# Performance work log

Measured on AMD Instinct MI355X. Metric: run time of the kernel, lower is better.

## Reference

```python
import jax, jax.numpy as jnp
import numpy as np

B, C, H_IMG, W_LEN = 32, 32, 16, 512
IN_CH = C * H_IMG          # 512, LSTM input size
OUT_CH = 1024              # bidirectional output size
HID = OUT_CH // 2          # 512, hidden per direction


def setup_inputs() -> dict:
    key = jax.random.key(0)
    ks = jax.random.split(key, 9)
    s = 1.0 / np.sqrt(HID)  # torch LSTM default init scale
    u = lambda k, shape: jax.random.uniform(k, shape, jnp.float32, -s, s)
    return {
        "x": jax.random.normal(ks[0], (B, C, H_IMG, W_LEN), jnp.float32),
        "W_ih_f": u(ks[1], (4 * HID, IN_CH)),
        "W_hh_f": u(ks[2], (4 * HID, HID)),
        "b_ih_f": u(ks[3], (4 * HID,)),
        "b_hh_f": u(ks[4], (4 * HID,)),
        "W_ih_b": u(ks[5], (4 * HID, IN_CH)),
        "W_hh_b": u(ks[6], (4 * HID, HID)),
        "b_ih_b": u(ks[7], (4 * HID,)),
        "b_hh_b": u(ks[8], (4 * HID,)),
    }


def _lstm_dir(x, W_ih, W_hh, b_ih, b_hh, reverse):
    # x: [B, T, IN] -> h sequence [B, T, HID]; torch gate order (i, f, g, o)
    xp = jnp.einsum('bti,gi->btg', x, W_ih) + b_ih + b_hh  # input proj for all steps
    xp = jnp.swapaxes(xp, 0, 1)  # [T, B, 4H]
    if reverse:
        xp = xp[::-1]
    h0 = jnp.zeros((x.shape[0], HID), x.dtype)

    def step(carry, xp_t):
        h, c = carry
        g = xp_t + h @ W_hh.T
        i, f, gg, o = jnp.split(g, 4, axis=-1)
        c = jax.nn.sigmoid(f) * c + jax.nn.sigmoid(i) * jnp.tanh(gg)
        h = jax.nn.sigmoid(o) * jnp.tanh(c)
        return (h, c), h

    _, hs = jax.lax.scan(step, (h0, h0), xp)  # hs: [T, B, HID]
    if reverse:
        hs = hs[::-1]
    return jnp.swapaxes(hs, 0, 1)  # [B, T, HID]


def reference(x, W_ih_f, W_hh_f, b_ih_f, b_hh_f, W_ih_b, W_hh_b, b_ih_b, b_hh_b):
    Bn, Cn, Hn, Wn = x.shape
    # permute(0,3,1,2).view(B, W, C*H): width is the time axis
    xs = jnp.transpose(x, (0, 3, 1, 2)).reshape(Bn, Wn, Cn * Hn)
    hf = _lstm_dir(xs, W_ih_f, W_hh_f, b_ih_f, b_hh_f, reverse=False)
    hb = _lstm_dir(xs, W_ih_b, W_hh_b, b_ih_b, b_hh_b, reverse=True)
    out = jnp.concatenate([hf, hb], axis=-1)        # [B, W, OUT]
    out = jnp.swapaxes(out, 1, 2)                    # [B, OUT, W]
    return out.reshape(Bn, -1, Hn, Wn)               # [B, OUT//H, H, W]
```

## Files before the change

### kernel.cpp

```cpp
#include <hip/hip_runtime.h>
#include <hip/hip_bf16.h>

#define BATCH 32
#define TLEN 512
#define INCH 512
#define HID 512

typedef __bf16 bf16x8 __attribute__((ext_vector_type(8)));
typedef float f32x4 __attribute__((ext_vector_type(4)));
typedef unsigned short u16x4 __attribute__((ext_vector_type(4)));
using bf16 = __hip_bfloat16;

#define OFF_XS2   0ull
#define OFF_WCAT  16777216ull
#define OFF_WHHP  20971520ull
#define OFF_BIAS  25165824ull
#define OFF_HBUF  25182208ull
#define OFF_CTR   25313280ull
#define OFF_FLAG  25313536ull
#define OFF_XP    25321728ull
#define WS_REQUIRED (25321728ull + 134217728ull)

__device__ __forceinline__ float sigmoid_fast(float x) {
    return 1.f / (1.f + __expf(-x));
}
__device__ __forceinline__ float tanh_fast(float x) {
    float ax = fabsf(x);
    float e = __expf(-2.f * ax);
    float r = (1.f - e) / (1.f + e);
    return copysignf(r, x);
}
__device__ __forceinline__ float bf2f(unsigned short u) {
    unsigned int i = ((unsigned int)u) << 16;
    float f; __builtin_memcpy(&f, &i, 4); return f;
}

__global__ void ws_too_small_kernel(float* out) {
    if (threadIdx.x == 0 && blockIdx.x == 0) out[0] = 12345.0f;
}

__global__ void pack_x_kernel(const float* __restrict__ x, bf16* __restrict__ XS2) {
    int bx = blockIdx.x;
    int b  = bx >> 6;
    int tt = (bx >> 3) & 7;
    int kt = bx & 7;
    __shared__ float tile[64][65];
    int tid  = threadIdx.x;
    int row2 = tid >> 6;
    int col  = tid & 63;
#pragma unroll
    for (int i = 0; i < 16; ++i) {
        int row = i * 4 + row2;
        int k = kt * 64 + row;
        tile[row][col] = x[((b * 32 + (k >> 4)) * 16 + (k & 15)) * 512 + tt * 64 + col];
    }
    __syncthreads();
#pragma unroll
    for (int i = 0; i < 16; ++i) {
        int trow = i * 4 + row2;
        int t = tt * 64 + trow;
        XS2[(t * 32 + b) * 512 + kt * 64 + col] = __float2bfloat16(tile[col][trow]);
    }
}

__global__ void pack_w_kernel(const float* __restrict__ Wih_f, const float* __restrict__ Whh_f,
                              const float* __restrict__ bih_f, const float* __restrict__ bhh_f,
                              const float* __restrict__ Wih_b, const float* __restrict__ Whh_b,
                              const float* __restrict__ bih_b, const float* __restrict__ bhh_b,
                              bf16* __restrict__ Wcat, bf16* __restrict__ Whhp,
                              float* __restrict__ bias, unsigned int* __restrict__ hbuf32,
                              unsigned int* __restrict__ ctr, unsigned int* __restrict__ flags) {
    long idx = (long)blockIdx.x * 256 + threadIdx.x;
    if (idx < 262144) {
        long e = idx * 8;
        int m = (int)(e >> 9), k = (int)(e & 511);
        const float* src = (m < 2048) ? &Wih_f[(long)m * 512 + k]
                                      : &Wih_b[(long)(m - 2048) * 512 + k];
        bf16* dst = &Wcat[e];
#pragma unroll
        for (int j = 0; j < 8; ++j) dst[j] = __float2bfloat16(src[j]);
        return;
    }
    idx -= 262144;
    if (idx < 262144) {
        long e = idx * 8;
        int k  = (int)(e & 511);
        int lm = (int)((e >> 9) & 63);
        int s  = (int)((e >> 15) & 31);
        int dir = (int)(e >> 20);
        int grow = (lm & 3) * 512 + s * 16 + (lm >> 2);
        const float* W = dir ? Whh_b : Whh_f;
        const float* src = &W[(long)grow * 512 + k];
        bf16* dst = &Whhp[e];
#pragma unroll
        for (int j = 0; j < 8; ++j) dst[j] = __float2bfloat16(src[j]);
        return;
    }
    idx -= 262144;
    if (idx < 4096) {
        int dir  = (int)(idx >> 11);
        int r    = (int)(idx & 2047);
        int s    = r >> 6, ul = (r >> 2) & 15, gate = r & 3;
        int g    = gate * 512 + s * 16 + ul;
        bias[idx] = (dir ? (bih_b[g] + bhh_b[g]) : (bih_f[g] + bhh_f[g]));
        return;
    }
    idx -= 4096;
    if (idx < 32768) { hbuf32[idx] = 0u; return; }
    idx -= 32768;
    if (idx < 64) { ctr[idx] = 0u; return; }
    idx -= 64;
    if (idx < 2048) { flags[idx] = 0u; return; }
}

__global__ __launch_bounds__(256, 2) void gemm_xp_kernel(const bf16* __restrict__ Wcat,
                                                         const bf16* __restrict__ XS2,
                                                         bf16* __restrict__ XP) {
    int bm = (blockIdx.x & 31) * 128;
    int bn = (blockIdx.x >> 5) * 128;
    __shared__ bf16 lA[128 * 40];
    __shared__ bf16 lB[128 * 40];
    int tid = threadIdx.x;
    int lane = tid & 63, w = tid >> 6;
    int wm = (w & 1) * 64, wn = (w >> 1) * 64;
    int fr = lane & 15, fq = lane >> 4;
    f32x4 acc[4][4] = {};
    int r = tid >> 2, c = tid & 3;
    for (int kt = 0; kt < 16; ++kt) {
        int k0 = kt * 32;
        *(bf16x8*)&lA[r * 40 + c * 8]        = *(const bf16x8*)&Wcat[(long)(bm + r) * 512 + k0 + c * 8];
        *(bf16x8*)&lA[(r + 64) * 40 + c * 8] = *(const bf16x8*)&Wcat[(long)(bm + r + 64) * 512 + k0 + c * 8];
        *(bf16x8*)&lB[r * 40 + c * 8]        = *(const bf16x8*)&XS2[(long)(bn + r) * 512 + k0 + c * 8];
        *(bf16x8*)&lB[(r + 64) * 40 + c * 8] = *(const bf16x8*)&XS2[(long)(bn + r + 64) * 512 + k0 + c * 8];
        __syncthreads();
        bf16x8 af[4], bfm[4];
#pragma unroll
        for (int i = 0; i < 4; ++i) af[i]  = *(const bf16x8*)&lA[(wm + i * 16 + fr) * 40 + fq * 8];
#pragma unroll
        for (int i = 0; i < 4; ++i) bfm[i] = *(const bf16x8*)&lB[(wn + i * 16 + fr) * 40 + fq * 8];
#pragma unroll
        for (int mi = 0; mi < 4; ++mi)
#pragma unroll
            for (int ni = 0; ni < 4; ++ni)
                acc[mi][ni] = __builtin_amdgcn_mfma_f32_16x16x32_bf16(af[mi], bfm[ni], acc[mi][ni], 0, 0, 0);
        __syncthreads();
    }
#pragma unroll
    for (int mi = 0; mi < 4; ++mi) {
#pragma unroll
        for (int rr = 0; rr < 4; ++rr) {
            int m = bm + wm + mi * 16 + fq * 4 + rr;
            int dir = m >> 11, cc = m & 2047;
            int gate = cc >> 9, u = cc & 511, s = u >> 4, ul = u & 15;
#pragma unroll
            for (int ni = 0; ni < 4; ++ni) {
                int n = bn + wn + ni * 16 + fr;
                int t = n >> 5, b = n & 31;
                long off = ((long)(t * 2 + dir) * 32 + s) * 2048 + (long)(ul * 32 + b) * 4 + gate;
                XP[off] = __float2bfloat16(acc[mi][ni][rr]);
            }
        }
    }
}

__global__ __launch_bounds__(512, 2) void lstm_rec_kernel(const bf16* __restrict__ Whhp,
                                                          const bf16* __restrict__ XP,
                                                          const float* __restrict__ bias,
                                                          bf16* hbuf, float* out,
                                                          unsigned int* flags) {
    int bx = blockIdx.x;
    int dir = bx >> 5, s = bx & 31;
    int tid = threadIdx.x;
    int lane = tid & 63, w = tid >> 6;
    int mt = w & 3, nt = w >> 2;
    int fr = lane & 15, fq = lane >> 4;
    __shared__ float obuf[16][512];
    __shared__ bf16  hstage[BATCH * 16];
    __shared__ bf16  hsh[32 * 520];
    __shared__ int   eps;

    const bf16* wbase = Whhp + ((long)((dir * 32 + s) * 64 + mt * 16 + fr)) * 512 + fq * 8;
    bf16x8 wA[16];
#pragma unroll
    for (int kt = 0; kt < 16; ++kt) wA[kt] = *(const bf16x8*)(wbase + kt * 32);

    int ul = mt * 4 + fq;
    int b  = nt * 16 + fr;
    f32x4 bv = *(const f32x4*)&bias[((dir * 32 + s) * 16 + ul) * 4];
    float cstate = 0.f;

    bf16* hb_dir = hbuf + (long)dir * 2 * 16384;
    unsigned int* myflag = flags + (dir * 32 + s) * 32;
    const unsigned int* pollflag = flags + (dir * 32 + (lane & 31)) * 32;
    float* outrow = out + (long)b * 524288 + (long)(dir * 512 + s * 16 + ul) * 512;
    int c0 = tid * 4;
    int sb0 = ((c0 >> 1) & 31) * 520 + (c0 >> 6) * 16;
    int sb1 = (((c0 + 2) >> 1) & 31) * 520 + (c0 >> 6) * 16;
    int guard = 1 << 21;

    if (tid == 0) eps = 0;
    __syncthreads();

    for (int t = 0; t < TLEN; ++t) {
        int ttime = dir ? (TLEN - 1 - t) : t;
        const bf16* xpp = XP + (long)(ttime * 2 + dir) * 65536 + s * 2048 + (ul * 32 + b) * 4;
        u16x4 xv = *(const u16x4*)xpp;

        if (t > 0) {
            if (w == 1) {
                unsigned int target = (unsigned int)t;
                for (;;) {
                    unsigned int v = __hip_atomic_load(pollflag, __ATOMIC_RELAXED,
                                                       __HIP_MEMORY_SCOPE_AGENT);
                    if (__all(v >= target)) break;
                    if (--guard <= 0) break;
                }
                if (lane == 0)
                    __hip_atomic_store(&eps, t, __ATOMIC_RELAXED,
                                       __HIP_MEMORY_SCOPE_WORKGROUP);
            } else {
                while (__hip_atomic_load(&eps, __ATOMIC_RELAXED,
                                         __HIP_MEMORY_SCOPE_WORKGROUP) < t) {
                    if (--guard <= 0) break;
                }
            }
        }

        {
            const bf16* src = hb_dir + (long)(t & 1) * 16384 + (long)tid * 32;
            f32x4 v0, v1, v2, v3;
            asm volatile(
                "global_load_dwordx4 %0, %4, off sc0 sc1\n\t"
                "global_load_dwordx4 %1, %4, off offset:16 sc0 sc1\n\t"
                "global_load_dwordx4 %2, %4, off offset:32 sc0 sc1\n\t"
                "global_load_dwordx4 %3, %4, off offset:48 sc0 sc1\n\t"
                "s_waitcnt vmcnt(0)"
                : "=&v"(v0), "=&v"(v1), "=&v"(v2), "=&v"(v3)
                : "v"(src) : "memory");
            bf16* d0 = &hsh[sb0];
            bf16* d1 = &hsh[sb1];
            *(f32x4*)(d0)     = v0;
            *(f32x4*)(d0 + 8) = v1;
            *(f32x4*)(d1)     = v2;
            *(f32x4*)(d1 + 8) = v3;
        }
        __syncthreads();

        f32x4 a0 = {}, a1 = {}, a2 = {}, a3 = {};
        const bf16* hrow = &hsh[(nt * 16 + fr) * 520 + fq * 8];
#pragma unroll
        for (int kt = 0; kt < 16; kt += 4) {
            bf16x8 h0 = *(const bf16x8*)(hrow + (kt + 0) * 32);
            bf16x8 h1 = *(const bf16x8*)(hrow + (kt + 1) * 32);
            bf16x8 h2 = *(const bf16x8*)(hrow + (kt + 2) * 32);
            bf16x8 h3 = *(const bf16x8*)(hrow + (kt + 3) * 32);
            a0 = __builtin_amdgcn_mfma_f32_16x16x32_bf16(wA[kt + 0], h0, a0, 0, 0, 0);
            a1 = __builtin_amdgcn_mfma_f32_16x16x32_bf16(wA[kt + 1], h1, a1, 0, 0, 0);
            a2 = __builtin_amdgcn_mfma_f32_16x16x32_bf16(wA[kt + 2], h2, a2, 0, 0, 0);
            a3 = __builtin_amdgcn_mfma_f32_16x16x32_bf16(wA[kt + 3], h3, a3, 0, 0, 0);
        }

        float gi = (a0[0] + a1[0]) + (a2[0] + a3[0]) + bv[0] + bf2f(xv.x);
        float gf = (a0[1] + a1[1]) + (a2[1] + a3[1]) + bv[1] + bf2f(xv.y);
        float gg = (a0[2] + a1[2]) + (a2[2] + a3[2]) + bv[2] + bf2f(xv.z);
        float go = (a0[3] + a1[3]) + (a2[3] + a3[3]) + bv[3] + bf2f(xv.w);
        float si = sigmoid_fast(gi), sf = sigmoid_fast(gf), so = sigmoid_fast(go);
        cstate = sf * cstate + si * tanh_fast(gg);
        float h = so * tanh_fast(cstate);

        hstage[b * 16 + ul] = __float2bfloat16(h);
        obuf[ttime & 15][tid] = h;
        __syncthreads();

        if (w == 0) {
            f32x4 hv = *(const f32x4*)&hstage[lane * 8];
            bf16* dst = hb_dir + (long)((t + 1) & 1) * 16384 + s * 512 + lane * 8;
            asm volatile("global_store_dwordx4 %0, %1, off sc0 sc1"
                         :: "v"(dst), "v"(hv) : "memory");
            asm volatile("s_waitcnt vmcnt(0)" ::: "memory");
            if (lane == 0)
                __hip_atomic_store(myflag, (unsigned int)(t + 1), __ATOMIC_RELAXED,
                                   __HIP_MEMORY_SCOPE_AGENT);
        }

        if ((t & 15) == 15) {
            int tb = ttime & ~15;
            float vals[16];
#pragma unroll
            for (int c = 0; c < 16; ++c) vals[c] = obuf[c][tid];
            float* op = outrow + tb;
#pragma unroll
            for (int c4 = 0; c4 < 4; ++c4)
                *(f32x4*)(op + c4 * 4) = *(f32x4*)&vals[c4 * 4];
        }
    }
}

extern "C" void kernel_launch(void* const* d_in, const int* in_sizes, int n_in,
                              void* d_out, int out_size, void* d_ws, size_t ws_size,
                              hipStream_t stream) {
    const float* x     = (const float*)d_in[0];
    const float* Wih_f = (const float*)d_in[1];
    const float* Whh_f = (const float*)d_in[2];
    const float* bih_f = (const float*)d_in[3];
    const float* bhh_f = (const float*)d_in[4];
    const float* Wih_b = (const float*)d_in[5];
    const float* Whh_b = (const float*)d_in[6];
    const float* bih_b = (const float*)d_in[7];
    const float* bhh_b = (const float*)d_in[8];
    float* out = (float*)d_out;

    if (ws_size < WS_REQUIRED) {
        ws_too_small_kernel<<<1, 64, 0, stream>>>(out);
        return;
    }

    char* ws = (char*)d_ws;
    bf16* XS2  = (bf16*)(ws + OFF_XS2);
    bf16* Wcat = (bf16*)(ws + OFF_WCAT);
    bf16* Whhp = (bf16*)(ws + OFF_WHHP);
    float* bias = (float*)(ws + OFF_BIAS);
    bf16* hbuf = (bf16*)(ws + OFF_HBUF);
    unsigned int* ctr   = (unsigned int*)(ws + OFF_CTR);
    unsigned int* flags = (unsigned int*)(ws + OFF_FLAG);
    bf16* XP   = (bf16*)(ws + OFF_XP);

    pack_x_kernel<<<2048, 256, 0, stream>>>(x, XS2);
    pack_w_kernel<<<2201, 256, 0, stream>>>(Wih_f, Whh_f, bih_f, bhh_f,
                                            Wih_b, Whh_b, bih_b, bhh_b,
                                            Wcat, Whhp, bias, (unsigned int*)hbuf, ctr, flags);
    gemm_xp_kernel<<<4096, 256, 0, stream>>>(Wcat, XS2, XP);
    lstm_rec_kernel<<<64, 512, 0, stream>>>(Whhp, XP, bias, hbuf, out, flags);
}
```

Measured before the change: 1.957 ms.

## Interleave forward and backward LSTM directions within each persistent workgroup

Merges the two direction workgroups into one, so 32 workgroups each keep both directions' recurrent weight slices in registers and alternate forward and backward steps. The goal is to hide each direction's cross-workgroup flag-polling latency behind the other direction's work, and to drop the single-wave poller plus LDS broadcast in favour of all waves polling directly. This doubles register use (launch bounds lowered to one block per SM) and LDS use. Each direction's steps are now serialized inside a single workgroup, which can lengthen the critical path if the overlap does not materialize.

```diff
diff --git a/kernel.cpp b/kernel.cpp
--- a/kernel.cpp
+++ b/kernel.cpp
@@ -163,135 +163,211 @@
     }
 }
 
-__global__ __launch_bounds__(512, 2) void lstm_rec_kernel(const bf16* __restrict__ Whhp,
+__global__ __launch_bounds__(512, 1) void lstm_rec_kernel(const bf16* __restrict__ Whhp,
                                                           const bf16* __restrict__ XP,
                                                           const float* __restrict__ bias,
                                                           bf16* hbuf, float* out,
                                                           unsigned int* flags) {
-    int bx = blockIdx.x;
-    int dir = bx >> 5, s = bx & 31;
+    int s = blockIdx.x;
     int tid = threadIdx.x;
     int lane = tid & 63, w = tid >> 6;
     int mt = w & 3, nt = w >> 2;
     int fr = lane & 15, fq = lane >> 4;
-    __shared__ float obuf[16][512];
-    __shared__ bf16  hstage[BATCH * 16];
-    __shared__ bf16  hsh[32 * 520];
-    __shared__ int   eps;
-
-    const bf16* wbase = Whhp + ((long)((dir * 32 + s) * 64 + mt * 16 + fr)) * 512 + fq * 8;
-    bf16x8 wA[16];
-#pragma unroll
-    for (int kt = 0; kt < 16; ++kt) wA[kt] = *(const bf16x8*)(wbase + kt * 32);
+    __shared__ float obuf[2][16][512];
+    __shared__ bf16  hstage[2][BATCH * 16];
+    __shared__ bf16  hsh[2][32 * 520];
+
+    const bf16* wbf = Whhp + ((long)((0 * 32 + s) * 64 + mt * 16 + fr)) * 512 + fq * 8;
+    const bf16* wbb = Whhp + ((long)((1 * 32 + s) * 64 + mt * 16 + fr)) * 512 + fq * 8;
+    bf16x8 wAf[16], wAb[16];
+#pragma unroll
+    for (int kt = 0; kt < 16; ++kt) wAf[kt] = *(const bf16x8*)(wbf + kt * 32);
+#pragma unroll
+    for (int kt = 0; kt < 16; ++kt) wAb[kt] = *(const bf16x8*)(wbb + kt * 32);
 
     int ul = mt * 4 + fq;
     int b  = nt * 16 + fr;
-    f32x4 bv = *(const f32x4*)&bias[((dir * 32 + s) * 16 + ul) * 4];
-    float cstate = 0.f;
-
-    bf16* hb_dir = hbuf + (long)dir * 2 * 16384;
-    unsigned int* myflag = flags + (dir * 32 + s) * 32;
-    const unsigned int* pollflag = flags + (dir * 32 + (lane & 31)) * 32;
-    float* outrow = out + (long)b * 524288 + (long)(dir * 512 + s * 16 + ul) * 512;
+    f32x4 bvf = *(const f32x4*)&bias[((0 * 32 + s) * 16 + ul) * 4];
+    f32x4 bvb = *(const f32x4*)&bias[((1 * 32 + s) * 16 + ul) * 4];
+    float csf = 0.f, csb = 0.f;
+
+    bf16* hb_f = hbuf;
+    bf16* hb_b = hbuf + 2 * 16384;
+    unsigned int* myflag_f = flags + (0 * 32 + s) * 32;
+    unsigned int* myflag_b = flags + (1 * 32 + s) * 32;
+    const unsigned int* pollf = flags + (0 * 32 + (lane & 31)) * 32;
+    const unsigned int* pollb = flags + (1 * 32 + (lane & 31)) * 32;
+    float* outrow_f = out + (long)b * 524288 + (long)(0 * 512 + s * 16 + ul) * 512;
+    float* outrow_b = out + (long)b * 524288 + (long)(1 * 512 + s * 16 + ul) * 512;
     int c0 = tid * 4;
     int sb0 = ((c0 >> 1) & 31) * 520 + (c0 >> 6) * 16;
     int sb1 = (((c0 + 2) >> 1) & 31) * 520 + (c0 >> 6) * 16;
     int guard = 1 << 21;
 
-    if (tid == 0) eps = 0;
-    __syncthreads();
-
     for (int t = 0; t < TLEN; ++t) {
-        int ttime = dir ? (TLEN - 1 - t) : t;
-        const bf16* xpp = XP + (long)(ttime * 2 + dir) * 65536 + s * 2048 + (ul * 32 + b) * 4;
-        u16x4 xv = *(const u16x4*)xpp;
-
-        if (t > 0) {
-            if (w == 1) {
+        {
+            int ttime = t;
+            const bf16* xpp = XP + (long)(ttime * 2 + 0) * 65536 + s * 2048 + (ul * 32 + b) * 4;
+            u16x4 xv = *(const u16x4*)xpp;
+
+            if (t > 0) {
                 unsigned int target = (unsigned int)t;
                 for (;;) {
-                    unsigned int v = __hip_atomic_load(pollflag, __ATOMIC_RELAXED,
+                    unsigned int v = __hip_atomic_load(pollf, __ATOMIC_RELAXED,
                                                        __HIP_MEMORY_SCOPE_AGENT);
                     if (__all(v >= target)) break;
                     if (--guard <= 0) break;
                 }
+            }
+            {
+                const bf16* src = hb_f + (long)(t & 1) * 16384 + (long)tid * 32;
+                f32x4 v0, v1, v2, v3;
+                asm volatile(
+                    "global_load_dwordx4 %0, %4, off sc0 sc1\n\t"
+                    "global_load_dwordx4 %1, %4, off offset:16 sc0 sc1\n\t"
+                    "global_load_dwordx4 %2, %4, off offset:32 sc0 sc1\n\t"
+                    "global_load_dwordx4 %3, %4, off offset:48 sc0 sc1\n\t"
+                    "s_waitcnt vmcnt(0)"
+                    : "=&v"(v0), "=&v"(v1), "=&v"(v2), "=&v"(v3)
+                    : "v"(src) : "memory");
+                bf16* d0 = &hsh[0][sb0];
+                bf16* d1 = &hsh[0][sb1];
+                *(f32x4*)(d0)     = v0;
+                *(f32x4*)(d0 + 8) = v1;
+                *(f32x4*)(d1)     = v2;
+                *(f32x4*)(d1 + 8) = v3;
+            }
+            __syncthreads();
+
+            f32x4 a0 = {}, a1 = {}, a2 = {}, a3 = {};
+            const bf16* hrow = &hsh[0][(nt * 16 + fr) * 520 + fq * 8];
+#pragma unroll
+            for (int kt = 0; kt < 16; kt += 4) {
+                bf16x8 h0 = *(const bf16x8*)(hrow + (kt + 0) * 32);
+                bf16x8 h1 = *(const bf16x8*)(hrow + (kt + 1) * 32);
+                bf16x8 h2 = *(const bf16x8*)(hrow + (kt + 2) * 32);
+                bf16x8 h3 = *(const bf16x8*)(hrow + (kt + 3) * 32);
+                a0 = __builtin_amdgcn_mfma_f32_16x16x32_bf16(wAf[kt + 0], h0, a0, 0, 0, 0);
+                a1 = __builtin_amdgcn_mfma_f32_16x16x32_bf16(wAf[kt + 1], h1, a1, 0, 0, 0);
+                a2 = __builtin_amdgcn_mfma_f32_16x16x32_bf16(wAf[kt + 2], h2, a2, 0, 0, 0);
+                a3 = __builtin_amdgcn_mfma_f32_16x16x32_bf16(wAf[kt + 3], h3, a3, 0, 0, 0);
+            }
+            float gi = (a0[0] + a1[0]) + (a2[0] + a3[0]) + bvf[0] + bf2f(xv.x);
+            float gf = (a0[1] + a1[1]) + (a2[1] + a3[1]) + bvf[1] + bf2f(xv.y);
+            float gg = (a0[2] + a1[2]) + (a2[2] + a3[2]) + bvf[2] + bf2f(xv.z);
+            float go = (a0[3] + a1[3]) + (a2[3] + a3[3]) + bvf[3] + bf2f(xv.w);
+            float si = sigmoid_fast(gi), sf = sigmoid_fast(gf), so = sigmoid_fast(go);
+            csf = sf * csf + si * tanh_fast(gg);
+            float h = so * tanh_fast(csf);
+
+            hstage[0][b * 16 + ul] = __float2bfloat16(h);
+            obuf[0][ttime & 15][tid] = h;
+            __syncthreads();
+
+            if (w == 0) {
+                f32x4 hv = *(const f32x4*)&hstage[0][lane * 8];
+                bf16* dst = hb_f + (long)((t + 1) & 1) * 16384 + s * 512 + lane * 8;
+                asm volatile("global_store_dwordx4 %0, %1, off sc0 sc1"
+                             :: "v"(dst), "v"(hv) : "memory");
+                asm volatile("s_waitcnt vmcnt(0)" ::: "memory");
                 if (lane == 0)
-                    __hip_atomic_store(&eps, t, __ATOMIC_RELAXED,
-                                       __HIP_MEMORY_SCOPE_WORKGROUP);
-            } else {
-                while (__hip_atomic_load(&eps, __ATOMIC_RELAXED,
-                                         __HIP_MEMORY_SCOPE_WORKGROUP) < t) {
+                    __hip_atomic_store(myflag_f, (unsigned int)(t + 1), __ATOMIC_RELAXED,
+                                       __HIP_MEMORY_SCOPE_AGENT);
+            }
+        }
+
+        {
+            int ttime = TLEN - 1 - t;
+            const bf16* xpp = XP + (long)(ttime * 2 + 1) * 65536 + s * 2048 + (ul * 32 + b) * 4;
+            u16x4 xv = *(const u16x4*)xpp;
+
+            if (t > 0) {
+                unsigned int target = (unsigned int)t;
+                for (;;) {
+                    unsigned int v = __hip_atomic_load(pollb, __ATOMIC_RELAXED,
+                                                       __HIP_MEMORY_SCOPE_AGENT);
+                    if (__all(v >= target)) break;
                     if (--guard <= 0) break;
                 }
             }
+            {
+                const bf16* src = hb_b + (long)(t & 1) * 16384 + (long)tid * 32;
+                f32x4 v0, v1, v2, v3;
+                asm volatile(
+                    "global_load_dwordx4 %0, %4, off sc0 sc1\n\t"
+                    "global_load_dwordx4 %1, %4, off offset:16 sc0 sc1\n\t"
+                    "global_load_dwordx4 %2, %4, off offset:32 sc0 sc1\n\t"
+                    "global_load_dwordx4 %3, %4, off offset:48 sc0 sc1\n\t"
+                    "s_waitcnt vmcnt(0)"
+                    : "=&v"(v0), "=&v"(v1), "=&v"(v2), "=&v"(v3)
+                    : "v"(src) : "memory");
+                bf16* d0 = &hsh[1][sb0];
+                bf16* d1 = &hsh[1][sb1];
+                *(f32x4*)(d0)     = v0;
+                *(f32x4*)(d0 + 8) = v1;
+                *(f32x4*)(d1)     = v2;
+                *(f32x4*)(d1 + 8) = v3;
+            }
+            __syncthreads();
+
+            f32x4 a0 = {}, a1 = {}, a2 = {}, a3 = {};
+            const bf16* hrow = &hsh[1][(nt * 16 + fr) * 520 + fq * 8];
+#pragma unroll
+            for (int kt = 0; kt < 16; kt += 4) {
+                bf16x8 h0 = *(const bf16x8*)(hrow + (kt + 0) * 32);
+                bf16x8 h1 = *(const bf16x8*)(hrow + (kt + 1) * 32);
+                bf16x8 h2 = *(const bf16x8*)(hrow + (kt + 2) * 32);
+                bf16x8 h3 = *(const bf16x8*)(hrow + (kt + 3) * 32);
+                a0 = __builtin_amdgcn_mfma_f32_16x16x32_bf16(wAb[kt + 0], h0, a0, 0, 0, 0);
+                a1 = __builtin_amdgcn_mfma_f32_16x16x32_bf16(wAb[kt + 1], h1, a1, 0, 0, 0);
+                a2 = __builtin_amdgcn_mfma_f32_16x16x32_bf16(wAb[kt + 2], h2, a2, 0, 0, 0);
+                a3 = __builtin_amdgcn_mfma_f32_16x16x32_bf16(wAb[kt + 3], h3, a3, 0, 0, 0);
+            }
+            float gi = (a0[0] + a1[0]) + (a2[0] + a3[0]) + bvb[0] + bf2f(xv.x);
+            float gf = (a0[1] + a1[1]) + (a2[1] + a3[1]) + bvb[1] + bf2f(xv.y);
+            float gg = (a0[2] + a1[2]) + (a2[2] + a3[2]) + bvb[2] + bf2f(xv.z);
+            float go = (a0[3] + a1[3]) + (a2[3] + a3[3]) + bvb[3] + bf2f(xv.w);
+            float si = sigmoid_fast(gi), sf = sigmoid_fast(gf), so = sigmoid_fast(go);
+            csb = sf * csb + si * tanh_fast(gg);
+            float h = so * tanh_fast(csb);
+
+            hstage[1][b * 16 + ul] = __float2bfloat16(h);
+            obuf[1][ttime & 15][tid] = h;
+            __syncthreads();
+
+            if (w == 0) {
+                f32x4 hv = *(const f32x4*)&hstage[1][lane * 8];
+                bf16* dst = hb_b + (long)((t + 1) & 1) * 16384 + s * 512 + lane * 8;
+                asm volatile("global_store_dwordx4 %0, %1, off sc0 sc1"
+                             :: "v"(dst), "v"(hv) : "memory");
+                asm volatile("s_waitcnt vmcnt(0)" ::: "memory");
+                if (lane == 0)
+                    __hip_atomic_store(myflag_b, (unsigned int)(t + 1), __ATOMIC_RELAXED,
+                                       __HIP_MEMORY_SCOPE_AGENT);
+            }
         }
 
-        {
-            const bf16* src = hb_dir + (long)(t & 1) * 16384 + (long)tid * 32;
-            f32x4 v0, v1, v2, v3;
-            asm volatile(
-                "global_load_dwordx4 %0, %4, off sc0 sc1\n\t"
-                "global_load_dwordx4 %1, %4, off offset:16 sc0 sc1\n\t"
-                "global_load_dwordx4 %2, %4, off offset:32 sc0 sc1\n\t"
-                "global_load_dwordx4 %3, %4, off offset:48 sc0 sc1\n\t"
-                "s_waitcnt vmcnt(0)"
-                : "=&v"(v0), "=&v"(v1), "=&v"(v2), "=&v"(v3)
-                : "v"(src) : "memory");
-            bf16* d0 = &hsh[sb0];
-            bf16* d1 = &hsh[sb1];
-            *(f32x4*)(d0)     = v0;
-            *(f32x4*)(d0 + 8) = v1;
-            *(f32x4*)(d1)     = v2;
-            *(f32x4*)(d1 + 8) = v3;
-        }
-        __syncthreads();
-
-        f32x4 a0 = {}, a1 = {}, a2 = {}, a3 = {};
-        const bf16* hrow = &hsh[(nt * 16 + fr) * 520 + fq * 8];
-#pragma unroll
-        for (int kt = 0; kt < 16; kt += 4) {
-            bf16x8 h0 = *(const bf16x8*)(hrow + (kt + 0) * 32);
-            bf16x8 h1 = *(const bf16x8*)(hrow + (kt + 1) * 32);
-            bf16x8 h2 = *(const bf16x8*)(hrow + (kt + 2) * 32);
-            bf16x8 h3 = *(const bf16x8*)(hrow + (kt + 3) * 32);
-            a0 = __builtin_amdgcn_mfma_f32_16x16x32_bf16(wA[kt + 0], h0, a0, 0, 0, 0);
-            a1 = __builtin_amdgcn_mfma_f32_16x16x32_bf16(wA[kt + 1], h1, a1, 0, 0, 0);
-            a2 = __builtin_amdgcn_mfma_f32_16x16x32_bf16(wA[kt + 2], h2, a2, 0, 0, 0);
-            a3 = __builtin_amdgcn_mfma_f32_16x16x32_bf16(wA[kt + 3], h3, a3, 0, 0, 0);
-        }
-
-        float gi = (a0[0] + a1[0]) + (a2[0] + a3[0]) + bv[0] + bf2f(xv.x);
-        float gf = (a0[1] + a1[1]) + (a2[1] + a3[1]) + bv[1] + bf2f(xv.y);
-        float gg = (a0[2] + a1[2]) + (a2[2] + a3[2]) + bv[2] + bf2f(xv.z);
-        float go = (a0[3] + a1[3]) + (a2[3] + a3[3]) + bv[3] + bf2f(xv.w);
-        float si = sigmoid_fast(gi), sf = sigmoid_fast(gf), so = sigmoid_fast(go);
-        cstate = sf * cstate + si * tanh_fast(gg);
-        float h = so * tanh_fast(cstate);
-
-        hstage[b * 16 + ul] = __float2bfloat16(h);
-        obuf[ttime & 15][tid] = h;
-        __syncthreads();
-
-        if (w == 0) {
-            f32x4 hv = *(const f32x4*)&hstage[lane * 8];
-            bf16* dst = hb_dir + (long)((t + 1) & 1) * 16384 + s * 512 + lane * 8;
-            asm volatile("global_store_dwordx4 %0, %1, off sc0 sc1"
-                         :: "v"(dst), "v"(hv) : "memory");
-            asm volatile("s_waitcnt vmcnt(0)" ::: "memory");
-            if (lane == 0)
-                __hip_atomic_store(myflag, (unsigned int)(t + 1), __ATOMIC_RELAXED,
-                                   __HIP_MEMORY_SCOPE_AGENT);
-        }
-
         if ((t & 15) == 15) {
-            int tb = ttime & ~15;
-            float vals[16];
-#pragma unroll
-            for (int c = 0; c < 16; ++c) vals[c] = obuf[c][tid];
-            float* op = outrow + tb;
-#pragma unroll
-            for (int c4 = 0; c4 < 4; ++c4)
-                *(f32x4*)(op + c4 * 4) = *(f32x4*)&vals[c4 * 4];
+            {
+                int tb = t & ~15;
+                float vals[16];
+#pragma unroll
+                for (int c = 0; c < 16; ++c) vals[c] = obuf[0][c][tid];
+                float* op = outrow_f + tb;
+#pragma unroll
+                for (int c4 = 0; c4 < 4; ++c4)
+                    *(f32x4*)(op + c4 * 4) = *(f32x4*)&vals[c4 * 4];
+            }
+            {
+                int tb = (TLEN - 1 - t) & ~15;
+                float vals[16];
+#pragma unroll
+                for (int c = 0; c < 16; ++c) vals[c] = obuf[1][c][tid];
+                float* op = outrow_b + tb;
+#pragma unroll
+                for (int c4 = 0; c4 < 4; ++c4)
+                    *(f32x4*)(op + c4 * 4) = *(f32x4*)&vals[c4 * 4];
+            }
         }
     }
 }
@@ -330,5 +406,5 @@
                                             Wih_b, Whh_b, bih_b, bhh_b,
                                             Wcat, Whhp, bias, (unsigned int*)hbuf, ctr, flags);
     gemm_xp_kernel<<<4096, 256, 0, stream>>>(Wcat, XS2, XP);
-    lstm_rec_kernel<<<64, 512, 0, stream>>>(Whhp, XP, bias, hbuf, out, flags);
-}
+    lstm_rec_kernel<<<32, 512, 0, stream>>>(Whhp, XP, bias, hbuf, out, flags);
+}
```

Result: slower. 2.991 ms (+52.8%).

## Halve recurrent LSTM workgroups, each handling two hidden slices for all batches

Applied to the files above, without the earlier changes.

The persistent recurrent kernel drops from 64 to 32 workgroups. Each workgroup now covers two 16-unit hidden slices across the full batch, where before it covered one slice. Each wave keeps its weight fragment and issues two MFMA chains, one per 16-row batch half, instead of splitting the batch across waves. This halves the number of flags polled per step and the cross-workgroup synchronisation fan-in, in exchange for more per-workgroup work and LDS, and the larger obuf lowers the occupancy bound to one workgroup per CU.

```diff
diff --git a/kernel.cpp b/kernel.cpp
--- a/kernel.cpp
+++ b/kernel.cpp
@@ -163,19 +163,20 @@
     }
 }
 
-__global__ __launch_bounds__(512, 2) void lstm_rec_kernel(const bf16* __restrict__ Whhp,
+__global__ __launch_bounds__(512, 1) void lstm_rec_kernel(const bf16* __restrict__ Whhp,
                                                           const bf16* __restrict__ XP,
                                                           const float* __restrict__ bias,
                                                           bf16* hbuf, float* out,
                                                           unsigned int* flags) {
     int bx = blockIdx.x;
-    int dir = bx >> 5, s = bx & 31;
+    int dir = bx >> 4, blk = bx & 15;
     int tid = threadIdx.x;
     int lane = tid & 63, w = tid >> 6;
-    int mt = w & 3, nt = w >> 2;
+    int mt = w & 3, su = w >> 2;
     int fr = lane & 15, fq = lane >> 4;
-    __shared__ float obuf[16][512];
-    __shared__ bf16  hstage[BATCH * 16];
+    int s = blk * 2 + su;
+    __shared__ float obuf[16][1024];
+    __shared__ bf16  hstage[32 * 32];
     __shared__ bf16  hsh[32 * 520];
     __shared__ int   eps;
 
@@ -184,18 +185,17 @@
 #pragma unroll
     for (int kt = 0; kt < 16; ++kt) wA[kt] = *(const bf16x8*)(wbase + kt * 32);
 
-    int ul = mt * 4 + fq;
-    int b  = nt * 16 + fr;
-    f32x4 bv = *(const f32x4*)&bias[((dir * 32 + s) * 16 + ul) * 4];
-    float cstate = 0.f;
+    int ul16 = mt * 4 + fq;
+    int ul32 = su * 16 + ul16;
+    f32x4 bv = *(const f32x4*)&bias[((dir * 32 + s) * 16 + ul16) * 4];
+    float cs0 = 0.f, cs1 = 0.f;
 
     bf16* hb_dir = hbuf + (long)dir * 2 * 16384;
-    unsigned int* myflag = flags + (dir * 32 + s) * 32;
-    const unsigned int* pollflag = flags + (dir * 32 + (lane & 31)) * 32;
-    float* outrow = out + (long)b * 524288 + (long)(dir * 512 + s * 16 + ul) * 512;
-    int c0 = tid * 4;
-    int sb0 = ((c0 >> 1) & 31) * 520 + (c0 >> 6) * 16;
-    int sb1 = (((c0 + 2) >> 1) & 31) * 520 + (c0 >> 6) * 16;
+    unsigned int* myflag = flags + (dir * 16 + blk) * 32;
+    const unsigned int* pollflag = flags + (dir * 16 + (lane & 15)) * 32;
+    float* outrow0 = out + (long)fr * 524288 + (long)(dir * 512 + s * 16 + ul16) * 512;
+    float* outrow1 = outrow0 + 16l * 524288;
+    int sbo = (tid & 31) * 520 + (tid >> 5) * 32;
     int guard = 1 << 21;
 
     if (tid == 0) eps = 0;
@@ -203,8 +203,9 @@
 
     for (int t = 0; t < TLEN; ++t) {
         int ttime = dir ? (TLEN - 1 - t) : t;
-        const bf16* xpp = XP + (long)(ttime * 2 + dir) * 65536 + s * 2048 + (ul * 32 + b) * 4;
-        u16x4 xv = *(const u16x4*)xpp;
+        const bf16* xpp = XP + (long)(ttime * 2 + dir) * 65536 + s * 2048 + (ul16 * 32 + fr) * 4;
+        u16x4 xv0 = *(const u16x4*)xpp;
+        u16x4 xv1 = *(const u16x4*)(xpp + 64);
 
         if (t > 0) {
             if (w == 1) {
@@ -237,47 +238,59 @@
                 "s_waitcnt vmcnt(0)"
                 : "=&v"(v0), "=&v"(v1), "=&v"(v2), "=&v"(v3)
                 : "v"(src) : "memory");
-            bf16* d0 = &hsh[sb0];
-            bf16* d1 = &hsh[sb1];
-            *(f32x4*)(d0)     = v0;
-            *(f32x4*)(d0 + 8) = v1;
-            *(f32x4*)(d1)     = v2;
-            *(f32x4*)(d1 + 8) = v3;
+            bf16* d = &hsh[sbo];
+            *(f32x4*)(d)      = v0;
+            *(f32x4*)(d + 8)  = v1;
+            *(f32x4*)(d + 16) = v2;
+            *(f32x4*)(d + 24) = v3;
         }
         __syncthreads();
 
         f32x4 a0 = {}, a1 = {}, a2 = {}, a3 = {};
-        const bf16* hrow = &hsh[(nt * 16 + fr) * 520 + fq * 8];
-#pragma unroll
-        for (int kt = 0; kt < 16; kt += 4) {
-            bf16x8 h0 = *(const bf16x8*)(hrow + (kt + 0) * 32);
-            bf16x8 h1 = *(const bf16x8*)(hrow + (kt + 1) * 32);
-            bf16x8 h2 = *(const bf16x8*)(hrow + (kt + 2) * 32);
-            bf16x8 h3 = *(const bf16x8*)(hrow + (kt + 3) * 32);
-            a0 = __builtin_amdgcn_mfma_f32_16x16x32_bf16(wA[kt + 0], h0, a0, 0, 0, 0);
-            a1 = __builtin_amdgcn_mfma_f32_16x16x32_bf16(wA[kt + 1], h1, a1, 0, 0, 0);
-            a2 = __builtin_amdgcn_mfma_f32_16x16x32_bf16(wA[kt + 2], h2, a2, 0, 0, 0);
-            a3 = __builtin_amdgcn_mfma_f32_16x16x32_bf16(wA[kt + 3], h3, a3, 0, 0, 0);
-        }
-
-        float gi = (a0[0] + a1[0]) + (a2[0] + a3[0]) + bv[0] + bf2f(xv.x);
-        float gf = (a0[1] + a1[1]) + (a2[1] + a3[1]) + bv[1] + bf2f(xv.y);
-        float gg = (a0[2] + a1[2]) + (a2[2] + a3[2]) + bv[2] + bf2f(xv.z);
-        float go = (a0[3] + a1[3]) + (a2[3] + a3[3]) + bv[3] + bf2f(xv.w);
-        float si = sigmoid_fast(gi), sf = sigmoid_fast(gf), so = sigmoid_fast(go);
-        cstate = sf * cstate + si * tanh_fast(gg);
-        float h = so * tanh_fast(cstate);
-
-        hstage[b * 16 + ul] = __float2bfloat16(h);
-        obuf[ttime & 15][tid] = h;
+        const bf16* hrow0 = &hsh[fr * 520 + fq * 8];
+        const bf16* hrow1 = &hsh[(16 + fr) * 520 + fq * 8];
+#pragma unroll
+        for (int kt = 0; kt < 16; kt += 2) {
+            bf16x8 h00 = *(const bf16x8*)(hrow0 + (kt + 0) * 32);
+            bf16x8 h01 = *(const bf16x8*)(hrow0 + (kt + 1) * 32);
+            bf16x8 h10 = *(const bf16x8*)(hrow1 + (kt + 0) * 32);
+            bf16x8 h11 = *(const bf16x8*)(hrow1 + (kt + 1) * 32);
+            a0 = __builtin_amdgcn_mfma_f32_16x16x32_bf16(wA[kt + 0], h00, a0, 0, 0, 0);
+            a2 = __builtin_amdgcn_mfma_f32_16x16x32_bf16(wA[kt + 0], h10, a2, 0, 0, 0);
+            a1 = __builtin_amdgcn_mfma_f32_16x16x32_bf16(wA[kt + 1], h01, a1, 0, 0, 0);
+            a3 = __builtin_amdgcn_mfma_f32_16x16x32_bf16(wA[kt + 1], h11, a3, 0, 0, 0);
+        }
+
+        float gi0 = a0[0] + a1[0] + bv[0] + bf2f(xv0.x);
+        float gf0 = a0[1] + a1[1] + bv[1] + bf2f(xv0.y);
+        float gg0 = a0[2] + a1[2] + bv[2] + bf2f(xv0.z);
+        float go0 = a0[3] + a1[3] + bv[3] + bf2f(xv0.w);
+        float gi1 = a2[0] + a3[0] + bv[0] + bf2f(xv1.x);
+        float gf1 = a2[1] + a3[1] + bv[1] + bf2f(xv1.y);
+        float gg1 = a2[2] + a3[2] + bv[2] + bf2f(xv1.z);
+        float go1 = a2[3] + a3[3] + bv[3] + bf2f(xv1.w);
+        float si0 = sigmoid_fast(gi0), sf0 = sigmoid_fast(gf0), so0 = sigmoid_fast(go0);
+        float si1 = sigmoid_fast(gi1), sf1 = sigmoid_fast(gf1), so1 = sigmoid_fast(go1);
+        cs0 = sf0 * cs0 + si0 * tanh_fast(gg0);
+        cs1 = sf1 * cs1 + si1 * tanh_fast(gg1);
+        float h0 = so0 * tanh_fast(cs0);
+        float h1 = so1 * tanh_fast(cs1);
+
+        hstage[fr * 32 + ul32]        = __float2bfloat16(h0);
+        hstage[(fr + 16) * 32 + ul32] = __float2bfloat16(h1);
+        obuf[ttime & 15][tid]       = h0;
+        obuf[ttime & 15][tid + 512] = h1;
         __syncthreads();
 
         if (w == 0) {
-            f32x4 hv = *(const f32x4*)&hstage[lane * 8];
-            bf16* dst = hb_dir + (long)((t + 1) & 1) * 16384 + s * 512 + lane * 8;
-            asm volatile("global_store_dwordx4 %0, %1, off sc0 sc1"
-                         :: "v"(dst), "v"(hv) : "memory");
-            asm volatile("s_waitcnt vmcnt(0)" ::: "memory");
+            f32x4 hv0 = *(const f32x4*)&hstage[lane * 16];
+            f32x4 hv1 = *(const f32x4*)&hstage[lane * 16 + 8];
+            bf16* dst = hb_dir + (long)((t + 1) & 1) * 16384 + blk * 1024 + lane * 16;
+            asm volatile(
+                "global_store_dwordx4 %0, %2, off sc0 sc1\n\t"
+                "global_store_dwordx4 %1, %3, off sc0 sc1\n\t"
+                "s_waitcnt vmcnt(0)"
+                :: "v"(dst), "v"(dst + 8), "v"(hv0), "v"(hv1) : "memory");
             if (lane == 0)
                 __hip_atomic_store(myflag, (unsigned int)(t + 1), __ATOMIC_RELAXED,
                                    __HIP_MEMORY_SCOPE_AGENT);
@@ -288,7 +301,13 @@
             float vals[16];
 #pragma unroll
             for (int c = 0; c < 16; ++c) vals[c] = obuf[c][tid];
-            float* op = outrow + tb;
+            float* op = outrow0 + tb;
+#pragma unroll
+            for (int c4 = 0; c4 < 4; ++c4)
+                *(f32x4*)(op + c4 * 4) = *(f32x4*)&vals[c4 * 4];
+#pragma unroll
+            for (int c = 0; c < 16; ++c) vals[c] = obuf[c][tid + 512];
+            op = outrow1 + tb;
 #pragma unroll
             for (int c4 = 0; c4 < 4; ++c4)
                 *(f32x4*)(op + c4 * 4) = *(f32x4*)&vals[c4 * 4];
@@ -330,5 +349,5 @@
                                             Wih_b, Whh_b, bih_b, bhh_b,
                                             Wcat, Whhp, bias, (unsigned int*)hbuf, ctr, flags);
     gemm_xp_kernel<<<4096, 256, 0, stream>>>(Wcat, XS2, XP);
-    lstm_rec_kernel<<<64, 512, 0, stream>>>(Whhp, XP, bias, hbuf, out, flags);
-}
+    lstm_rec_kernel<<<32, 512, 0, stream>>>(Whhp, XP, bias, hbuf, out, flags);
+}
```

New measurement: 2.421 ms. 1.24x slower.

## Replace block barrier with per-slice LDS counters for fine-grained h dependency tracking

Applied to the files above, without the earlier changes.

Every thread now polls the global flag of the producer slice it loads instead of one wave polling all flags and broadcasting through LDS. The h tile is double-buffered in LDS, and per-slice workgroup-scope counters replace the __syncthreads before the MFMA loop. Each wave starts its K loop at a slice-dependent offset and waits only for the specific k-chunk it needs, so compute can begin as soon as the first producers' data arrive. This trades one barrier for many LDS atomic polls and more global polling traffic. Launch bounds change to one block per SM to make room for the doubled LDS.

```diff
diff --git a/kernel.cpp b/kernel.cpp
--- a/kernel.cpp
+++ b/kernel.cpp
@@ -163,7 +163,7 @@
     }
 }
 
-__global__ __launch_bounds__(512, 2) void lstm_rec_kernel(const bf16* __restrict__ Whhp,
+__global__ __launch_bounds__(512, 1) void lstm_rec_kernel(const bf16* __restrict__ Whhp,
                                                           const bf16* __restrict__ XP,
                                                           const float* __restrict__ bias,
                                                           bf16* hbuf, float* out,
@@ -176,8 +176,10 @@
     int fr = lane & 15, fq = lane >> 4;
     __shared__ float obuf[16][512];
     __shared__ bf16  hstage[BATCH * 16];
-    __shared__ bf16  hsh[32 * 520];
-    __shared__ int   eps;
+    __shared__ bf16  hsh[2][32 * 520];
+    __shared__ unsigned int scnt[2][32];
+
+    if (tid < 64) scnt[tid >> 5][tid & 31] = 0u;
 
     const bf16* wbase = Whhp + ((long)((dir * 32 + s) * 64 + mt * 16 + fr)) * 512 + fq * 8;
     bf16x8 wA[16];
@@ -191,43 +193,30 @@
 
     bf16* hb_dir = hbuf + (long)dir * 2 * 16384;
     unsigned int* myflag = flags + (dir * 32 + s) * 32;
-    const unsigned int* pollflag = flags + (dir * 32 + (lane & 31)) * 32;
+    int p = tid >> 4;
+    const unsigned int* pflag = flags + (dir * 32 + p) * 32;
     float* outrow = out + (long)b * 524288 + (long)(dir * 512 + s * 16 + ul) * 512;
     int c0 = tid * 4;
     int sb0 = ((c0 >> 1) & 31) * 520 + (c0 >> 6) * 16;
     int sb1 = (((c0 + 2) >> 1) & 31) * 520 + (c0 >> 6) * 16;
+    int kt_base = ((s >> 1) + 1) & 15;
     int guard = 1 << 21;
 
-    if (tid == 0) eps = 0;
     __syncthreads();
 
     for (int t = 0; t < TLEN; ++t) {
         int ttime = dir ? (TLEN - 1 - t) : t;
+        int buf = t & 1;
         const bf16* xpp = XP + (long)(ttime * 2 + dir) * 65536 + s * 2048 + (ul * 32 + b) * 4;
         u16x4 xv = *(const u16x4*)xpp;
 
-        if (t > 0) {
-            if (w == 1) {
-                unsigned int target = (unsigned int)t;
-                for (;;) {
-                    unsigned int v = __hip_atomic_load(pollflag, __ATOMIC_RELAXED,
-                                                       __HIP_MEMORY_SCOPE_AGENT);
-                    if (__all(v >= target)) break;
-                    if (--guard <= 0) break;
-                }
-                if (lane == 0)
-                    __hip_atomic_store(&eps, t, __ATOMIC_RELAXED,
-                                       __HIP_MEMORY_SCOPE_WORKGROUP);
-            } else {
-                while (__hip_atomic_load(&eps, __ATOMIC_RELAXED,
-                                         __HIP_MEMORY_SCOPE_WORKGROUP) < t) {
-                    if (--guard <= 0) break;
-                }
+        {
+            unsigned int target = (unsigned int)t;
+            while (__hip_atomic_load(pflag, __ATOMIC_RELAXED,
+                                     __HIP_MEMORY_SCOPE_AGENT) < target) {
+                if (--guard <= 0) break;
             }
-        }
-
-        {
-            const bf16* src = hb_dir + (long)(t & 1) * 16384 + (long)tid * 32;
+            const bf16* src = hb_dir + (long)buf * 16384 + (long)tid * 32;
             f32x4 v0, v1, v2, v3;
             asm volatile(
                 "global_load_dwordx4 %0, %4, off sc0 sc1\n\t"
@@ -237,27 +226,35 @@
                 "s_waitcnt vmcnt(0)"
                 : "=&v"(v0), "=&v"(v1), "=&v"(v2), "=&v"(v3)
                 : "v"(src) : "memory");
-            bf16* d0 = &hsh[sb0];
-            bf16* d1 = &hsh[sb1];
+            bf16* d0 = &hsh[buf][sb0];
+            bf16* d1 = &hsh[buf][sb1];
             *(f32x4*)(d0)     = v0;
             *(f32x4*)(d0 + 8) = v1;
             *(f32x4*)(d1)     = v2;
             *(f32x4*)(d1 + 8) = v3;
-        }
-        __syncthreads();
-
+            __hip_atomic_fetch_add(&scnt[buf][p], 1u, __ATOMIC_RELEASE,
+                                   __HIP_MEMORY_SCOPE_WORKGROUP);
+        }
+
+        unsigned int starget = 16u * ((unsigned int)(t >> 1) + 1u);
         f32x4 a0 = {}, a1 = {}, a2 = {}, a3 = {};
-        const bf16* hrow = &hsh[(nt * 16 + fr) * 520 + fq * 8];
-#pragma unroll
-        for (int kt = 0; kt < 16; kt += 4) {
-            bf16x8 h0 = *(const bf16x8*)(hrow + (kt + 0) * 32);
-            bf16x8 h1 = *(const bf16x8*)(hrow + (kt + 1) * 32);
-            bf16x8 h2 = *(const bf16x8*)(hrow + (kt + 2) * 32);
-            bf16x8 h3 = *(const bf16x8*)(hrow + (kt + 3) * 32);
-            a0 = __builtin_amdgcn_mfma_f32_16x16x32_bf16(wA[kt + 0], h0, a0, 0, 0, 0);
-            a1 = __builtin_amdgcn_mfma_f32_16x16x32_bf16(wA[kt + 1], h1, a1, 0, 0, 0);
-            a2 = __builtin_amdgcn_mfma_f32_16x16x32_bf16(wA[kt + 2], h2, a2, 0, 0, 0);
-            a3 = __builtin_amdgcn_mfma_f32_16x16x32_bf16(wA[kt + 3], h3, a3, 0, 0, 0);
+        const bf16* hrow = &hsh[buf][(nt * 16 + fr) * 520 + fq * 8];
+#pragma unroll
+        for (int j = 0; j < 16; ++j) {
+            int kt = (kt_base + j) & 15;
+            while (__hip_atomic_load(&scnt[buf][2 * kt], __ATOMIC_ACQUIRE,
+                                     __HIP_MEMORY_SCOPE_WORKGROUP) < starget) {
+                if (--guard <= 0) break;
+            }
+            while (__hip_atomic_load(&scnt[buf][2 * kt + 1], __ATOMIC_ACQUIRE,
+                                     __HIP_MEMORY_SCOPE_WORKGROUP) < starget) {
+                if (--guard <= 0) break;
+            }
+            bf16x8 hB = *(const bf16x8*)(hrow + kt * 32);
+            if ((j & 3) == 0)      a0 = __builtin_amdgcn_mfma_f32_16x16x32_bf16(wA[kt], hB, a0, 0, 0, 0);
+            else if ((j & 3) == 1) a1 = __builtin_amdgcn_mfma_f32_16x16x32_bf16(wA[kt], hB, a1, 0, 0, 0);
+            else if ((j & 3) == 2) a2 = __builtin_amdgcn_mfma_f32_16x16x32_bf16(wA[kt], hB, a2, 0, 0, 0);
+            else                   a3 = __builtin_amdgcn_mfma_f32_16x16x32_bf16(wA[kt], hB, a3, 0, 0, 0);
         }
 
         float gi = (a0[0] + a1[0]) + (a2[0] + a3[0]) + bv[0] + bf2f(xv.x);
```

New measurement: 3.570 ms. 1.82x slower.
